# Optimization experiments

Measured on AMD Instinct MI355X. Metric: run time of the kernel, lower is better.

The kernel has to match this reference:

```python
import jax, jax.numpy as jnp
import numpy as np

N_BATCH, C, H, W = 4, 256, 64, 64

def setup_inputs() -> dict:
    key = jax.random.key(0)
    ks = jax.random.split(key, 6)
    scale = 1.0 / np.sqrt(C)  # kaiming-ish init for 1x1 convs
    x = jax.random.normal(ks[0], (N_BATCH, C, H, W), dtype=jnp.float32)
    Wg = jax.random.normal(ks[1], (C, C), dtype=jnp.float32) * scale
    Wt = jax.random.normal(ks[2], (C, C), dtype=jnp.float32) * scale
    Wp = jax.random.normal(ks[3], (C, C), dtype=jnp.float32) * scale
    Wo = jax.random.normal(ks[4], (C, C), dtype=jnp.float32) * scale
    z = jnp.zeros((C,), dtype=jnp.float32)
    return {"x": x, "Wg": Wg, "bg": z, "Wt": Wt, "bt": z,
            "Wp": Wp, "bp": z, "Wo": Wo, "bo": z}

def reference(x, Wg, bg, Wt, bt, Wp, bp, Wo, bo):
    n, c, h, w = x.shape
    # 1x1 convs == per-position linear over channels; flatten spatial -> (n, N, c)
    xf = x.reshape(n, c, h * w).transpose(0, 2, 1)
    g_x = xf @ Wg.T + bg          # (n, N, c)
    theta_x = xf @ Wt.T + bt      # (n, N, c)
    phi_x = xf @ Wp.T + bp        # (n, N, c)
    # unscaled embedded-gaussian attention: softmax(theta @ phi^T)
    logits = jnp.einsum('nqc,nkc->nqk', theta_x, phi_x)  # (n, N, N)
    pw = jax.nn.softmax(logits, axis=-1)
    y = jnp.einsum('nqk,nkc->nqc', pw, g_x)              # (n, N, c)
    out = y @ Wo.T + bo                                  # conv_out (1x1)
    return x + out.transpose(0, 2, 1).reshape(n, c, h, w)
```

## Files before the change

### kernel.cpp

```cpp
#include <hip/hip_runtime.h>
#include <math.h>

#define CDIM 256
#define SDIM 4096
#define NBATCH 4

typedef _Float16 f16;
typedef _Float16 f16x4 __attribute__((ext_vector_type(4)));
typedef _Float16 f16x8 __attribute__((ext_vector_type(8)));
typedef float    f32x16 __attribute__((ext_vector_type(16)));

union PK2 { f16 h[2]; unsigned u; };
union CV8 { f16x8 v; uint2 q[2]; };

__device__ __forceinline__ void gload_lds16(const f16* gp, void* lp) {
    __builtin_amdgcn_global_load_lds(
        (const __attribute__((address_space(1))) void*)gp,
        (__attribute__((address_space(3))) void*)lp, 16, 0, 0);
}


__global__ __launch_bounds__(256, 2)
void proj_kernel(const float* __restrict__ x,
                 const float* __restrict__ Wt, const float* __restrict__ bt,
                 const float* __restrict__ Wp, const float* __restrict__ bp,
                 const float* __restrict__ Wg, const float* __restrict__ bg,
                 f16* __restrict__ theta_t, f16* __restrict__ phi_t,
                 f16* __restrict__ g_out)
{
    const int p = blockIdx.z % 3;
    const int n = blockIdx.z / 3;
    const float* W    = (p == 0) ? Wt : (p == 1) ? Wp : Wg;
    const float* bias = (p == 0) ? bt : (p == 1) ? bp : bg;
    const float* xb = x + (size_t)n * CDIM * SDIM;
    const int s0 = blockIdx.x * 128;
    const int m0 = blockIdx.y * 128;

    __shared__ __align__(16) char smraw[34816];
    unsigned (*xs)[128][34] = reinterpret_cast<unsigned (*)[128][34]>(smraw);
    f16 (*tr)[136]          = reinterpret_cast<f16 (*)[136]>(smraw);

    const int t = threadIdx.x, w = t >> 6, l = t & 63, ln = l & 31, hi = l >> 5;
    const int wm = w & 1, wn = w >> 1;

    f16x8 aW[2][16];
    #pragma unroll
    for (int mt = 0; mt < 2; ++mt) {
        const float* wr = W + (size_t)(m0 + 64 * wm + 32 * mt + ln) * CDIM + 8 * hi;
        #pragma unroll
        for (int j = 0; j < 16; ++j) {
            float4 u0 = *(const float4*)(wr + 16 * j);
            float4 u1 = *(const float4*)(wr + 16 * j + 4);
            f16x8 v;
            v[0] = (f16)u0.x; v[1] = (f16)u0.y; v[2] = (f16)u0.z; v[3] = (f16)u0.w;
            v[4] = (f16)u1.x; v[5] = (f16)u1.y; v[6] = (f16)u1.z; v[7] = (f16)u1.w;
            aW[mt][j] = v;
        }
    }

    f32x16 acc[2][2];
    #pragma unroll
    for (int a = 0; a < 2; ++a)
        #pragma unroll
        for (int b = 0; b < 2; ++b)
            #pragma unroll
            for (int r = 0; r < 16; ++r) acc[a][b][r] = 0.0f;

    const int sL = t & 127;
    const int kB = (t >> 7) * 32;

    float xv[32];
#define PLOAD(k0)                                                             \
    { _Pragma("unroll")                                                       \
      for (int i = 0; i < 32; ++i)                                            \
          xv[i] = xb[(size_t)((k0) + kB + i) * SDIM + s0 + sL]; }
#define PWRITE(b)                                                             \
    { _Pragma("unroll")                                                       \
      for (int m = 0; m < 16; ++m) {                                          \
          PK2 pk; pk.h[0] = (f16)xv[2 * m]; pk.h[1] = (f16)xv[2 * m + 1];     \
          xs[b][sL][(kB >> 1) + m] = pk.u; } }

    PLOAD(0);
    for (int ci = 0; ci < 4; ++ci) {
        const int b = ci & 1;
        PWRITE(b);
        __syncthreads();
        if (ci < 3) PLOAD((ci + 1) * 64);
        #pragma unroll
        for (int j = 0; j < 4; ++j) {
            f16x8 bx[2];
            #pragma unroll
            for (int nt = 0; nt < 2; ++nt) {
                const unsigned* pr = &xs[b][64 * wn + 32 * nt + ln][8 * j + 4 * hi];
                f16x4 lo = *(const f16x4*)pr;
                f16x4 h4 = *(const f16x4*)(pr + 2);
                f16x8 bb;
                bb[0]=lo[0]; bb[1]=lo[1]; bb[2]=lo[2]; bb[3]=lo[3];
                bb[4]=h4[0]; bb[5]=h4[1]; bb[6]=h4[2]; bb[7]=h4[3];
                bx[nt] = bb;
            }
            #pragma unroll
            for (int mt = 0; mt < 2; ++mt)
                #pragma unroll
                for (int nt = 0; nt < 2; ++nt)
                    acc[mt][nt] = __builtin_amdgcn_mfma_f32_32x32x16_f16(
                        aW[mt][ci * 4 + j], bx[nt], acc[mt][nt], 0, 0, 0);
        }
    }
#undef PLOAD
#undef PWRITE

    float bv[2][16];
    #pragma unroll
    for (int mt = 0; mt < 2; ++mt)
        #pragma unroll
        for (int r = 0; r < 16; ++r)
            bv[mt][r] = bias[m0 + 64 * wm + 32 * mt + (r & 3) + 8 * (r >> 2) + 4 * hi];

    __syncthreads();
    if (p < 2) {
        #pragma unroll
        for (int mt = 0; mt < 2; ++mt)
            #pragma unroll
            for (int nt = 0; nt < 2; ++nt)
                #pragma unroll
                for (int r = 0; r < 16; ++r)
                    tr[64 * wn + 32 * nt + ln]
                      [64 * wm + 32 * mt + (r & 3) + 8 * (r >> 2) + 4 * hi] =
                        (f16)(acc[mt][nt][r] + bv[mt][r]);
        __syncthreads();
        f16* out = ((p == 0) ? theta_t : phi_t) + (size_t)n * SDIM * CDIM;
        const int row = t >> 1, ch = (t & 1) * 64;
        #pragma unroll
        for (int i = 0; i < 8; ++i)
            *(f16x8*)&out[(size_t)(s0 + row) * CDIM + m0 + ch + 8 * i] =
                *(const f16x8*)&tr[row][ch + 8 * i];
    } else {
        f16* out = g_out + (size_t)n * CDIM * SDIM;
        #pragma unroll
        for (int mt = 0; mt < 2; ++mt)
            #pragma unroll
            for (int nt = 0; nt < 2; ++nt)
                #pragma unroll
                for (int r = 0; r < 16; ++r)
                    out[(size_t)(m0 + 64 * wm + 32 * mt + (r & 3) + 8 * (r >> 2) + 4 * hi)
                        * SDIM + s0 + 64 * wn + 32 * nt + ln] =
                        (f16)(acc[mt][nt][r] + bv[mt][r]);
    }
}

__global__ __launch_bounds__(256, 2)
void attn_kernel(const f16* __restrict__ theta,
                 const f16* __restrict__ phi,
                 const f16* __restrict__ g,
                 f16* __restrict__ Op,
                 float* __restrict__ pm,
                 float* __restrict__ pl)
{
    const int bx    = blockIdx.x;
    const int n     = bx >> 5;
    const int q0    = (bx & 31) * 128;
    const int split = blockIdx.y;
    const int koff  = split * (SDIM / 4);
    const int NCH   = (SDIM / 4) / 32;

    __shared__ f16x8 bufP[2][1024];
    __shared__ f16x8 bufG[2][1024];

    const int t  = threadIdx.x;
    const int w  = t >> 6;
    const int l  = t & 63;
    const int ln = l & 31;
    const int hi = l >> 5;

    const f16* thb = theta + (size_t)n * SDIM * CDIM;
    const f16* phb = phi   + (size_t)n * SDIM * CDIM;
    const f16* gb  = g     + (size_t)n * CDIM * SDIM;

    const int myq = q0 + 32 * w + ln;

    f16x8 bT[16];
    {
        const f16* ap = thb + (size_t)myq * CDIM + hi * 8;
        #pragma unroll
        for (int j = 0; j < 16; ++j)
            bT[j] = *(const f16x8*)(ap + 16 * j);
    }

    f32x16 O[8];
    #pragma unroll
    for (int ct = 0; ct < 8; ++ct)
        #pragma unroll
        for (int r = 0; r < 16; ++r) O[ct][r] = 0.0f;

    float m_run = -INFINITY, l_run = 0.0f;

#define ISSUE_CHUNK(k0, b)                                                    \
    {                                                                         \
        _Pragma("unroll")                                                     \
        for (int it = 0; it < 4; ++it) {                                      \
            const int slot = w * 256 + it * 64 + l;                           \
            const int key  = slot >> 5;                                       \
            const int grp  = (slot & 31) ^ key;                               \
            gload_lds16(phb + (size_t)((k0) + key) * CDIM + grp * 8,          \
                        &bufP[b][w * 256 + it * 64]);                         \
        }                                                                     \
        _Pragma("unroll")                                                     \
        for (int it = 0; it < 4; ++it) {                                      \
            const int slot = w * 256 + it * 64 + l;                           \
            const int chan = slot >> 2;                                       \
            const int kg   = (slot & 3) ^ (chan & 3) ^ ((chan >> 2) & 3);     \
            gload_lds16(gb + (size_t)chan * SDIM + (k0) + kg * 8,             \
                        &bufG[b][w * 256 + it * 64]);                         \
        }                                                                     \
    }

    ISSUE_CHUNK(koff, 0);

    for (int ci = 0; ci < NCH; ++ci) {
        const int b = ci & 1;
        __syncthreads();
        if (ci + 1 < NCH) ISSUE_CHUNK(koff + (ci + 1) * 32, b ^ 1);

        f32x16 sC;
        #pragma unroll
        for (int r = 0; r < 16; ++r) sC[r] = 0.0f;
        #pragma unroll
        for (int j = 0; j < 16; ++j) {
            const int grp = 2 * j + hi;
            f16x8 a = bufP[b][ln * 32 + (grp ^ ln)];
            sC = __builtin_amdgcn_mfma_f32_32x32x16_f16(a, bT[j], sC, 0, 0, 0);
        }

        float mx = sC[0];
        #pragma unroll
        for (int r = 1; r < 16; ++r) mx = fmaxf(mx, sC[r]);
        mx = fmaxf(mx, __shfl_xor(mx, 32));
        const float mn = fmaxf(m_run, mx);
        const float al = __expf(m_run - mn);
        m_run = mn;
        float sum = 0.0f;
        #pragma unroll
        for (int r = 0; r < 16; ++r) {
            sC[r] = __expf(sC[r] - mn);
            sum += sC[r];
        }
        sum += __shfl_xor(sum, 32);
        l_run = l_run * al + sum;

        if (__any(al != 1.0f)) {
            #pragma unroll
            for (int ct = 0; ct < 8; ++ct)
                #pragma unroll
                for (int r = 0; r < 16; ++r) O[ct][r] *= al;
        }

        f16x8 pf[2];
        #pragma unroll
        for (int ks = 0; ks < 2; ++ks) {
            #pragma unroll
            for (int j = 0; j < 4; ++j) {
                const float own = hi ? sC[8 * ks + 4 + j] : sC[8 * ks + j];
                const float oth = hi ? sC[8 * ks + j]     : sC[8 * ks + 4 + j];
                const float par = __shfl_xor(oth, 32);
                pf[ks][j]     = (f16)(hi ? par : own);
                pf[ks][4 + j] = (f16)(hi ? own : par);
            }
        }

        #pragma unroll
        for (int ks = 0; ks < 2; ++ks) {
            const int kg = 2 * ks + hi;
            #pragma unroll
            for (int ct = 0; ct < 8; ++ct) {
                const int chan = 32 * ct + ln;
                f16x8 ga = bufG[b][chan * 4 + (kg ^ (ln & 3) ^ ((ln >> 2) & 3))];
                O[ct] = __builtin_amdgcn_mfma_f32_32x32x16_f16(ga, pf[ks], O[ct], 0, 0, 0);
            }
        }
    }
#undef ISSUE_CHUNK

    __syncthreads();
    {
        f16* tw = (f16*)bufP + (size_t)w * 1152;
        f16* Opb = Op + ((size_t)(split * NBATCH + n)) * SDIM * CDIM;
        const int q  = l >> 1;
        const int ch = (l & 1) * 16;
        #pragma unroll
        for (int ct = 0; ct < 8; ++ct) {
            #pragma unroll
            for (int q4 = 0; q4 < 4; ++q4) {
                f16x4 v;
                v[0] = (f16)O[ct][4 * q4 + 0];
                v[1] = (f16)O[ct][4 * q4 + 1];
                v[2] = (f16)O[ct][4 * q4 + 2];
                v[3] = (f16)O[ct][4 * q4 + 3];
                *(f16x4*)&tw[ln * 36 + 8 * q4 + 4 * hi] = v;
            }
            f16x4 r0 = *(const f16x4*)&tw[q * 36 + ch + 0];
            f16x4 r1 = *(const f16x4*)&tw[q * 36 + ch + 4];
            f16x4 r2 = *(const f16x4*)&tw[q * 36 + ch + 8];
            f16x4 r3 = *(const f16x4*)&tw[q * 36 + ch + 12];
            f16x8 o0, o1;
            o0[0]=r0[0]; o0[1]=r0[1]; o0[2]=r0[2]; o0[3]=r0[3];
            o0[4]=r1[0]; o0[5]=r1[1]; o0[6]=r1[2]; o0[7]=r1[3];
            o1[0]=r2[0]; o1[1]=r2[1]; o1[2]=r2[2]; o1[3]=r2[3];
            o1[4]=r3[0]; o1[5]=r3[1]; o1[6]=r3[2]; o1[7]=r3[3];
            f16* dst = Opb + (size_t)(q0 + 32 * w + q) * CDIM + 32 * ct + ch;
            *(f16x8*)(dst)     = o0;
            *(f16x8*)(dst + 8) = o1;
        }
        if (hi == 0) {
            pm[(size_t)(split * NBATCH + n) * SDIM + myq] = m_run;
            pl[(size_t)(split * NBATCH + n) * SDIM + myq] = l_run;
        }
    }
}

__global__ __launch_bounds__(256, 2)
void outproj_kernel(const f16* __restrict__ Op,
                    const float* __restrict__ pm,
                    const float* __restrict__ pl,
                    const float* __restrict__ Wo,
                    const float* __restrict__ bo,
                    const float* __restrict__ x,
                    float* __restrict__ out)
{
    const int n  = blockIdx.z;
    const int s0 = blockIdx.x * 128;
    const int m0 = blockIdx.y * 128;

    __shared__ __align__(16) unsigned ys[2][128][34];
    __shared__ float scs[4][128];

    const int t = threadIdx.x, w = t >> 6, l = t & 63, ln = l & 31, hi = l >> 5;
    const int wm = w & 1, wn = w >> 1;

    if (t < 128) {
        const int s = s0 + t;
        float mv[4], lv[4];
        float M = -INFINITY;
        #pragma unroll
        for (int i = 0; i < 4; ++i) {
            mv[i] = pm[((size_t)i * NBATCH + n) * SDIM + s];
            lv[i] = pl[((size_t)i * NBATCH + n) * SDIM + s];
            M = fmaxf(M, mv[i]);
        }
        float d = 0.0f, e[4];
        #pragma unroll
        for (int i = 0; i < 4; ++i) { e[i] = __expf(mv[i] - M); d += e[i] * lv[i]; }
        const float rd = 1.0f / d;
        #pragma unroll
        for (int i = 0; i < 4; ++i) scs[i][t] = e[i] * rd;
    }

    f16x8 aW[2][16];
    #pragma unroll
    for (int mt = 0; mt < 2; ++mt) {
        const float* wr = Wo + (size_t)(m0 + 64 * wm + 32 * mt + ln) * CDIM + 8 * hi;
        #pragma unroll
        for (int j = 0; j < 16; ++j) {
            float4 u0 = *(const float4*)(wr + 16 * j);
            float4 u1 = *(const float4*)(wr + 16 * j + 4);
            f16x8 v;
            v[0] = (f16)u0.x; v[1] = (f16)u0.y; v[2] = (f16)u0.z; v[3] = (f16)u0.w;
            v[4] = (f16)u1.x; v[5] = (f16)u1.y; v[6] = (f16)u1.z; v[7] = (f16)u1.w;
            aW[mt][j] = v;
        }
    }

    f32x16 acc[2][2];
    #pragma unroll
    for (int a = 0; a < 2; ++a)
        #pragma unroll
        for (int b = 0; b < 2; ++b)
            #pragma unroll
            for (int r = 0; r < 16; ++r) acc[a][b][r] = 0.0f;

    const f16* Opb[4];
    #pragma unroll
    for (int i = 0; i < 4; ++i)
        Opb[i] = Op + ((size_t)i * NBATCH + n) * SDIM * CDIM;

    __syncthreads();

    f16x8 yv[4];
#define OLOAD(k0)                                                             \
    { _Pragma("unroll")                                                       \
      for (int u4 = 0; u4 < 4; ++u4) {                                        \
          const int u = u4 * 256 + t;                                         \
          const int kg = u & 7, sl = u >> 3;                                  \
          const size_t off = (size_t)(s0 + sl) * CDIM + (k0) + 8 * kg;        \
          f16x8 a0 = *(const f16x8*)(Opb[0] + off);                           \
          f16x8 a1 = *(const f16x8*)(Opb[1] + off);                           \
          f16x8 a2 = *(const f16x8*)(Opb[2] + off);                           \
          f16x8 a3 = *(const f16x8*)(Opb[3] + off);                           \
          const float c0 = scs[0][sl], c1 = scs[1][sl];                       \
          const float c2 = scs[2][sl], c3 = scs[3][sl];                       \
          f16x8 r;                                                            \
          _Pragma("unroll")                                                   \
          for (int e = 0; e < 8; ++e)                                         \
              r[e] = (f16)(c0 * (float)a0[e] + c1 * (float)a1[e] +            \
                           c2 * (float)a2[e] + c3 * (float)a3[e]);            \
          yv[u4] = r; } }
#define OWRITE(b)                                                             \
    { _Pragma("unroll")                                                       \
      for (int u4 = 0; u4 < 4; ++u4) {                                        \
          const int u = u4 * 256 + t;                                         \
          const int kg = u & 7, sl = u >> 3;                                  \
          CV8 cv; cv.v = yv[u4];                                              \
          *(uint2*)&ys[b][sl][4 * kg]     = cv.q[0];                          \
          *(uint2*)&ys[b][sl][4 * kg + 2] = cv.q[1]; } }

    OLOAD(0);
    for (int ci = 0; ci < 4; ++ci) {
        const int b = ci & 1;
        OWRITE(b);
        __syncthreads();
        if (ci < 3) OLOAD((ci + 1) * 64);
        #pragma unroll
        for (int j = 0; j < 4; ++j) {
            f16x8 bx[2];
            #pragma unroll
            for (int nt = 0; nt < 2; ++nt) {
                const unsigned* pr = &ys[b][64 * wn + 32 * nt + ln][8 * j + 4 * hi];
                f16x4 lo = *(const f16x4*)pr;
                f16x4 h4 = *(const f16x4*)(pr + 2);
                f16x8 bb;
                bb[0]=lo[0]; bb[1]=lo[1]; bb[2]=lo[2]; bb[3]=lo[3];
                bb[4]=h4[0]; bb[5]=h4[1]; bb[6]=h4[2]; bb[7]=h4[3];
                bx[nt] = bb;
            }
            #pragma unroll
            for (int mt = 0; mt < 2; ++mt)
                #pragma unroll
                for (int nt = 0; nt < 2; ++nt)
                    acc[mt][nt] = __builtin_amdgcn_mfma_f32_32x32x16_f16(
                        aW[mt][ci * 4 + j], bx[nt], acc[mt][nt], 0, 0, 0);
        }
    }
#undef OLOAD
#undef OWRITE

    const float* xb = x + (size_t)n * CDIM * SDIM;
    float* ob = out + (size_t)n * CDIM * SDIM;
    #pragma unroll
    for (int mt = 0; mt < 2; ++mt)
        #pragma unroll
        for (int r = 0; r < 16; ++r) {
            const int c = m0 + 64 * wm + 32 * mt + (r & 3) + 8 * (r >> 2) + 4 * hi;
            const float bv = bo[c];
            #pragma unroll
            for (int nt = 0; nt < 2; ++nt) {
                const size_t idx = (size_t)c * SDIM + s0 + 64 * wn + 32 * nt + ln;
                ob[idx] = acc[mt][nt][r] + bv + xb[idx];
            }
        }
}

extern "C" void kernel_launch(void* const* d_in, const int* in_sizes, int n_in,
                              void* d_out, int out_size, void* d_ws, size_t ws_size,
                              hipStream_t stream)
{
    const float* x  = (const float*)d_in[0];
    const float* Wg = (const float*)d_in[1];
    const float* bg = (const float*)d_in[2];
    const float* Wt = (const float*)d_in[3];
    const float* bt = (const float*)d_in[4];
    const float* Wp = (const float*)d_in[5];
    const float* bp = (const float*)d_in[6];
    const float* Wo = (const float*)d_in[7];
    const float* bo = (const float*)d_in[8];

    const size_t half_buf = (size_t)NBATCH * CDIM * SDIM * sizeof(f16);
    const size_t mlbuf    = (size_t)4 * NBATCH * SDIM * sizeof(float);
    char* wsb = (char*)d_ws;
    f16*   theta = (f16*)(wsb);
    f16*   phi   = (f16*)(wsb + half_buf);
    f16*   g     = (f16*)(wsb + 2 * half_buf);
    f16*   Op    = (f16*)(wsb + 3 * half_buf);
    float* pm    = (float*)(wsb + 7 * half_buf);
    float* pl    = (float*)(wsb + 7 * half_buf + mlbuf);
    float* out   = (float*)d_out;

    proj_kernel<<<dim3(SDIM / 128, CDIM / 128, NBATCH * 3), 256, 0, stream>>>(
        x, Wt, bt, Wp, bp, Wg, bg, theta, phi, g);
    attn_kernel<<<dim3(NBATCH * (SDIM / 128), 4), 256, 0, stream>>>(
        theta, phi, g, Op, pm, pl);
    outproj_kernel<<<dim3(SDIM / 128, CDIM / 128, NBATCH), 256, 0, stream>>>(
        Op, pm, pl, Wo, bo, x, out);
}
```

Before: 254.0 us.

## Stage projection stores through LDS, lazy softmax rescale, halve outproj tile width

The g projection now goes through the shared transpose buffer so its global stores become coalesced 16-byte rows, and theta/phi stores are remapped so each row gets contiguous vector writes. The attention kernel only raises the running max when the new max exceeds it by more than a threshold of 4, which skips most O rescales. That relies on exp values up to e^4 staying in range, which is safe in fp32 but changes the numerics slightly. The output projection uses 64-column spatial tiles, doubling its grid for more occupancy at the cost of loading the Wo fragments twice as often.

```diff
diff --git a/kernel.cpp b/kernel.cpp
--- a/kernel.cpp
+++ b/kernel.cpp
@@ -130,22 +130,34 @@
                         (f16)(acc[mt][nt][r] + bv[mt][r]);
         __syncthreads();
         f16* out = ((p == 0) ? theta_t : phi_t) + (size_t)n * SDIM * CDIM;
-        const int row = t >> 1, ch = (t & 1) * 64;
-        #pragma unroll
-        for (int i = 0; i < 8; ++i)
-            *(f16x8*)&out[(size_t)(s0 + row) * CDIM + m0 + ch + 8 * i] =
-                *(const f16x8*)&tr[row][ch + 8 * i];
+        #pragma unroll
+        for (int ps = 0; ps < 8; ++ps) {
+            const int id  = ps * 256 + t;
+            const int row = id >> 4;
+            const int c8  = id & 15;
+            *(f16x8*)&out[(size_t)(s0 + row) * CDIM + m0 + c8 * 8] =
+                *(const f16x8*)&tr[row][c8 * 8];
+        }
     } else {
-        f16* out = g_out + (size_t)n * CDIM * SDIM;
         #pragma unroll
         for (int mt = 0; mt < 2; ++mt)
             #pragma unroll
             for (int nt = 0; nt < 2; ++nt)
                 #pragma unroll
                 for (int r = 0; r < 16; ++r)
-                    out[(size_t)(m0 + 64 * wm + 32 * mt + (r & 3) + 8 * (r >> 2) + 4 * hi)
-                        * SDIM + s0 + 64 * wn + 32 * nt + ln] =
+                    tr[64 * wm + 32 * mt + (r & 3) + 8 * (r >> 2) + 4 * hi]
+                      [64 * wn + 32 * nt + ln] =
                         (f16)(acc[mt][nt][r] + bv[mt][r]);
+        __syncthreads();
+        f16* out = g_out + (size_t)n * CDIM * SDIM;
+        #pragma unroll
+        for (int ps = 0; ps < 8; ++ps) {
+            const int id  = ps * 256 + t;
+            const int row = id >> 4;
+            const int s8  = id & 15;
+            *(f16x8*)&out[(size_t)(m0 + row) * SDIM + s0 + s8 * 8] =
+                *(const f16x8*)&tr[row][s8 * 8];
+        }
     }
 }
 
@@ -236,7 +248,7 @@
         #pragma unroll
         for (int r = 1; r < 16; ++r) mx = fmaxf(mx, sC[r]);
         mx = fmaxf(mx, __shfl_xor(mx, 32));
-        const float mn = fmaxf(m_run, mx);
+        const float mn = (mx > m_run + 4.0f) ? mx : m_run;
         const float al = __expf(m_run - mn);
         m_run = mn;
         float sum = 0.0f;
@@ -328,16 +340,16 @@
                     float* __restrict__ out)
 {
     const int n  = blockIdx.z;
-    const int s0 = blockIdx.x * 128;
+    const int s0 = blockIdx.x * 64;
     const int m0 = blockIdx.y * 128;
 
-    __shared__ __align__(16) unsigned ys[2][128][34];
-    __shared__ float scs[4][128];
+    __shared__ __align__(16) unsigned ys[2][64][34];
+    __shared__ float scs[4][64];
 
     const int t = threadIdx.x, w = t >> 6, l = t & 63, ln = l & 31, hi = l >> 5;
     const int wm = w & 1, wn = w >> 1;
 
-    if (t < 128) {
+    if (t < 64) {
         const int s = s0 + t;
         float mv[4], lv[4];
         float M = -INFINITY;
@@ -370,13 +382,11 @@
         }
     }
 
-    f32x16 acc[2][2];
+    f32x16 acc[2];
     #pragma unroll
     for (int a = 0; a < 2; ++a)
         #pragma unroll
-        for (int b = 0; b < 2; ++b)
-            #pragma unroll
-            for (int r = 0; r < 16; ++r) acc[a][b][r] = 0.0f;
+        for (int r = 0; r < 16; ++r) acc[a][r] = 0.0f;
 
     const f16* Opb[4];
     #pragma unroll
@@ -385,11 +395,11 @@
 
     __syncthreads();
 
-    f16x8 yv[4];
+    f16x8 yv[2];
 #define OLOAD(k0)                                                             \
     { _Pragma("unroll")                                                       \
-      for (int u4 = 0; u4 < 4; ++u4) {                                        \
-          const int u = u4 * 256 + t;                                         \
+      for (int u2 = 0; u2 < 2; ++u2) {                                        \
+          const int u = u2 * 256 + t;                                         \
           const int kg = u & 7, sl = u >> 3;                                  \
           const size_t off = (size_t)(s0 + sl) * CDIM + (k0) + 8 * kg;        \
           f16x8 a0 = *(const f16x8*)(Opb[0] + off);                           \
@@ -403,13 +413,13 @@
           for (int e = 0; e < 8; ++e)                                         \
               r[e] = (f16)(c0 * (float)a0[e] + c1 * (float)a1[e] +            \
                            c2 * (float)a2[e] + c3 * (float)a3[e]);            \
-          yv[u4] = r; } }
+          yv[u2] = r; } }
 #define OWRITE(b)                                                             \
     { _Pragma("unroll")                                                       \
-      for (int u4 = 0; u4 < 4; ++u4) {                                        \
-          const int u = u4 * 256 + t;                                         \
+      for (int u2 = 0; u2 < 2; ++u2) {                                        \
+          const int u = u2 * 256 + t;                                         \
           const int kg = u & 7, sl = u >> 3;                                  \
-          CV8 cv; cv.v = yv[u4];                                              \
+          CV8 cv; cv.v = yv[u2];                                              \
           *(uint2*)&ys[b][sl][4 * kg]     = cv.q[0];                          \
           *(uint2*)&ys[b][sl][4 * kg + 2] = cv.q[1]; } }
 
@@ -421,23 +431,16 @@
         if (ci < 3) OLOAD((ci + 1) * 64);
         #pragma unroll
         for (int j = 0; j < 4; ++j) {
-            f16x8 bx[2];
-            #pragma unroll
-            for (int nt = 0; nt < 2; ++nt) {
-                const unsigned* pr = &ys[b][64 * wn + 32 * nt + ln][8 * j + 4 * hi];
-                f16x4 lo = *(const f16x4*)pr;
-                f16x4 h4 = *(const f16x4*)(pr + 2);
-                f16x8 bb;
-                bb[0]=lo[0]; bb[1]=lo[1]; bb[2]=lo[2]; bb[3]=lo[3];
-                bb[4]=h4[0]; bb[5]=h4[1]; bb[6]=h4[2]; bb[7]=h4[3];
-                bx[nt] = bb;
-            }
+            const unsigned* pr = &ys[b][32 * wn + ln][8 * j + 4 * hi];
+            f16x4 lo = *(const f16x4*)pr;
+            f16x4 h4 = *(const f16x4*)(pr + 2);
+            f16x8 bb;
+            bb[0]=lo[0]; bb[1]=lo[1]; bb[2]=lo[2]; bb[3]=lo[3];
+            bb[4]=h4[0]; bb[5]=h4[1]; bb[6]=h4[2]; bb[7]=h4[3];
             #pragma unroll
             for (int mt = 0; mt < 2; ++mt)
-                #pragma unroll
-                for (int nt = 0; nt < 2; ++nt)
-                    acc[mt][nt] = __builtin_amdgcn_mfma_f32_32x32x16_f16(
-                        aW[mt][ci * 4 + j], bx[nt], acc[mt][nt], 0, 0, 0);
+                acc[mt] = __builtin_amdgcn_mfma_f32_32x32x16_f16(
+                    aW[mt][ci * 4 + j], bb, acc[mt], 0, 0, 0);
         }
     }
 #undef OLOAD
@@ -451,11 +454,8 @@
         for (int r = 0; r < 16; ++r) {
             const int c = m0 + 64 * wm + 32 * mt + (r & 3) + 8 * (r >> 2) + 4 * hi;
             const float bv = bo[c];
-            #pragma unroll
-            for (int nt = 0; nt < 2; ++nt) {
-                const size_t idx = (size_t)c * SDIM + s0 + 64 * wn + 32 * nt + ln;
-                ob[idx] = acc[mt][nt][r] + bv + xb[idx];
-            }
+            const size_t idx = (size_t)c * SDIM + s0 + 32 * wn + ln;
+            ob[idx] = acc[mt][r] + bv + xb[idx];
         }
 }
 
@@ -488,6 +488,6 @@
         x, Wt, bt, Wp, bp, Wg, bg, theta, phi, g);
     attn_kernel<<<dim3(NBATCH * (SDIM / 128), 4), 256, 0, stream>>>(
         theta, phi, g, Op, pm, pl);
-    outproj_kernel<<<dim3(SDIM / 128, CDIM / 128, NBATCH), 256, 0, stream>>>(
+    outproj_kernel<<<dim3(SDIM / 64, CDIM / 128, NBATCH), 256, 0, stream>>>(
         Op, pm, pl, Wo, bo, x, out);
 }
```

Result: no change. 250.4 us (-1.4%).
